# Performance work log

Hardware: AMD Instinct MI355X
Metric: run time of the kernel (lower is better)

Reference implementation:

```python
import jax, jax.numpy as jnp
import numpy as np

BINS = 10
MMT = 0.9
N = 33554432  # 2^25 elements


def setup_inputs() -> dict:
    key = jax.random.key(0)
    k1, k2, k3 = jax.random.split(key, 3)
    pred = jax.random.normal(k1, (N,), dtype=jnp.float32)
    target = jax.random.randint(k2, (N,), 0, 2, dtype=jnp.int32)
    acc_sum = jax.random.uniform(k3, (BINS,), dtype=jnp.float32)
    return {"pred": pred, "target": target, "acc_sum": acc_sum}


def reference(pred, target, acc_sum):
    bins = acc_sum.shape[0]
    # border = arange(bins+1)/bins, with last edge nudged up by 1e-6
    border = jnp.arange(bins + 1, dtype=jnp.float32) / bins
    border = border.at[-1].add(1e-6)

    t = target.astype(jnp.float32)
    # gradient density measure on detached predictions
    g = jnp.abs(jax.nn.sigmoid(jax.lax.stop_gradient(pred)) - t)
    # bin index: g in [border[i], border[i+1])  ->  i
    idx = jnp.clip(jnp.searchsorted(border, g, side='right') - 1, 0, bins - 1)

    # single-pass histogram (replaces the per-bin mask loop)
    counts = jax.ops.segment_sum(jnp.ones_like(g), idx, num_segments=bins)
    nonempty = counts > 0

    # momentum-accumulated bin statistics (only updated for non-empty bins)
    acc_new = jnp.where(nonempty, MMT * acc_sum + (1.0 - MMT) * counts, acc_sum)

    tot = jnp.float32(max(pred.shape[0], 1.0))
    safe_acc = jnp.where(nonempty, acc_new, 1.0)
    bin_w = jnp.where(nonempty, tot / safe_acc, 0.0)  # [bins]

    n = jnp.sum(nonempty.astype(jnp.float32))
    bin_w = jnp.where(n > 0, bin_w / jnp.maximum(n, 1.0), bin_w)

    # per-element GHM weights are constants w.r.t. pred (buffer + detached g)
    w = jax.lax.stop_gradient(bin_w[idx])

    # BCE-with-logits, numerically stable
    bce = jnp.maximum(pred, 0.0) - pred * t + jnp.log1p(jnp.exp(-jnp.abs(pred)))
    return jnp.sum(w * bce) / tot
```

## Files before the change

kernel.cpp:

```cpp
#include <hip/hip_runtime.h>

#define BINS 10
#define NTHREADS 256


__device__ __forceinline__ float wave_reduce_add(float v) {
#pragma unroll
    for (int off = 32; off > 0; off >>= 1) v += __shfl_down(v, off, 64);
    return v;
}
__device__ __forceinline__ unsigned int wave_reduce_addu(unsigned int v) {
#pragma unroll
    for (int off = 32; off > 0; off >>= 1) v += __shfl_down((int)v, off, 64);
    return v;
}

#define GHM_C1  2.19722458f
#define GHM_C2  1.38629436f
#define GHM_C3  0.84729786f
#define GHM_C4  0.40546511f
#define GHM_C5  0.0f
#define GHM_C6 -0.40546511f
#define GHM_C7 -0.84729786f
#define GHM_C8 -1.38629436f
#define GHM_C9 -2.19722458f
#define LOG2E 1.44269504f

__global__ __launch_bounds__(NTHREADS, 8) void ghm_pass1(
    const float* __restrict__ pred, const int* __restrict__ target,
    float* __restrict__ g_T,
    unsigned int* __restrict__ g_C,
    int n4, int n)
{
    float T[BINS];
    unsigned int cnt[BINS];
#pragma unroll
    for (int b = 0; b < BINS; ++b) { T[b] = 0.f; cnt[b] = 0u; }

    const float4* __restrict__ p4 = reinterpret_cast<const float4*>(pred);
    const int4*   __restrict__ t4 = reinterpret_cast<const int4*>(target);

    const int tid    = threadIdx.x;
    const int gtid   = blockIdx.x * NTHREADS + tid;
    const int stride = gridDim.x * NTHREADS;
    const int step   = 2 * stride;

#define GHM_BODY(xv, tv)                                                     \
    {                                                                        \
        const float xs_[4] = {(xv).x, (xv).y, (xv).z, (xv).w};               \
        const int   ts_[4] = {(tv).x, (tv).y, (tv).z, (tv).w};               \
        _Pragma("unroll")                                                    \
        for (int j = 0; j < 4; ++j) {                                        \
            const float x = xs_[j];                                          \
            const float y = (ts_[j] != 0) ? x : -x;                          \
            const float E = __builtin_amdgcn_exp2f(-y * LOG2E);              \
            const float bce2 = __builtin_amdgcn_logf(1.0f + E);              \
            T[0] += bce2;                                                    \
            { const bool p = (y <= GHM_C1); T[1]+=p?bce2:0.f; cnt[1]+=p; }   \
            { const bool p = (y <= GHM_C2); T[2]+=p?bce2:0.f; cnt[2]+=p; }   \
            { const bool p = (y <= GHM_C3); T[3]+=p?bce2:0.f; cnt[3]+=p; }   \
            { const bool p = (y <= GHM_C4); T[4]+=p?bce2:0.f; cnt[4]+=p; }   \
            { const bool p = (y <= GHM_C5); T[5]+=p?bce2:0.f; cnt[5]+=p; }   \
            { const bool p = (y <= GHM_C6); T[6]+=p?bce2:0.f; cnt[6]+=p; }   \
            { const bool p = (y <= GHM_C7); T[7]+=p?bce2:0.f; cnt[7]+=p; }   \
            { const bool p = (y <= GHM_C8); T[8]+=p?bce2:0.f; cnt[8]+=p; }   \
            { const bool p = (y <= GHM_C9); T[9]+=p?bce2:0.f; cnt[9]+=p; }   \
        }                                                                    \
    }

    const int R = (step > 0) ? (n4 / step) : 0;
    if (R > 0) {
        int idx = gtid;
        float4 xa0 = p4[idx];
        int4   ta0 = t4[idx];
        float4 xa1 = p4[idx + stride];
        int4   ta1 = t4[idx + stride];
        for (int r = 1; r < R; ++r) {
            const int nidx = gtid + r * step;
            const float4 xb0 = p4[nidx];
            const int4   tb0 = t4[nidx];
            const float4 xb1 = p4[nidx + stride];
            const int4   tb1 = t4[nidx + stride];
            GHM_BODY(xa0, ta0);
            GHM_BODY(xa1, ta1);
            xa0 = xb0; ta0 = tb0; xa1 = xb1; ta1 = tb1;
        }
        GHM_BODY(xa0, ta0);
        GHM_BODY(xa1, ta1);
    }
    for (int i = gtid + R * step; i < n4; i += stride) {
        const float4 xv = p4[i];
        const int4   tv = t4[i];
        GHM_BODY(xv, tv);
    }
    if (gtid == 0) {
        for (int i = n4 * 4; i < n; ++i) {
            const float x = pred[i];
            const float y = (target[i] != 0) ? x : -x;
            const float E = __builtin_amdgcn_exp2f(-y * LOG2E);
            const float bce2 = __builtin_amdgcn_logf(1.0f + E);
            T[0] += bce2;
            { const bool p = (y <= GHM_C1); T[1]+=p?bce2:0.f; cnt[1]+=p; }
            { const bool p = (y <= GHM_C2); T[2]+=p?bce2:0.f; cnt[2]+=p; }
            { const bool p = (y <= GHM_C3); T[3]+=p?bce2:0.f; cnt[3]+=p; }
            { const bool p = (y <= GHM_C4); T[4]+=p?bce2:0.f; cnt[4]+=p; }
            { const bool p = (y <= GHM_C5); T[5]+=p?bce2:0.f; cnt[5]+=p; }
            { const bool p = (y <= GHM_C6); T[6]+=p?bce2:0.f; cnt[6]+=p; }
            { const bool p = (y <= GHM_C7); T[7]+=p?bce2:0.f; cnt[7]+=p; }
            { const bool p = (y <= GHM_C8); T[8]+=p?bce2:0.f; cnt[8]+=p; }
            { const bool p = (y <= GHM_C9); T[9]+=p?bce2:0.f; cnt[9]+=p; }
        }
    }
#undef GHM_BODY

    __shared__ float        r_T[BINS];
    __shared__ unsigned int r_C[BINS];
    if (tid < BINS) { r_T[tid] = 0.f; r_C[tid] = 0u; }
    __syncthreads();

    const int lane = tid & 63;
#pragma unroll
    for (int b = 0; b < BINS; ++b) {
        const float        v = wave_reduce_add(T[b]);
        const unsigned int c = (b > 0) ? wave_reduce_addu(cnt[b]) : 0u;
        if (lane == 0) {
            atomicAdd(&r_T[b], v);
            if (b > 0) atomicAdd(&r_C[b], c);
        }
    }
    __syncthreads();

    if (tid < BINS) {
        atomicAdd(&g_T[tid], r_T[tid]);
        atomicAdd(&g_C[tid], r_C[tid]);
    }
}

__global__ void ghm_finalize(const float* __restrict__ g_T,
                             const unsigned int* __restrict__ g_C,
                             const float* __restrict__ acc_sum,
                             float* __restrict__ out, float tot, unsigned int ntot)
{
    if (threadIdx.x == 0 && blockIdx.x == 0) {
        const float LN2 = 0.69314718056f;
        float S[BINS];
        float cntf[BINS];
#pragma unroll
        for (int b = 0; b < BINS; ++b) {
            const float        Tc = g_T[b];
            const float        Tn = (b + 1 < BINS) ? g_T[b + 1] : 0.f;
            const unsigned int Cc = (b == 0) ? ntot : g_C[b];
            const unsigned int Cn = (b + 1 < BINS) ? g_C[b + 1] : 0u;
            S[b]    = (Tc - Tn) * LN2;
            cntf[b] = (float)(Cc - Cn);
        }
        float binw[BINS];
        int nne = 0;
#pragma unroll
        for (int b = 0; b < BINS; ++b) {
            const bool ne = (cntf[b] > 0.0f);
            const float accn = ne ? (0.9f * acc_sum[b] + 0.1f * cntf[b]) : acc_sum[b];
            binw[b] = ne ? (tot / accn) : 0.0f;
            nne += ne ? 1 : 0;
        }
        const float scale = (nne > 0) ? (1.0f / (float)nne) : 1.0f;
        float res = 0.0f;
#pragma unroll
        for (int b = 0; b < BINS; ++b) res += (binw[b] * scale) * S[b];
        out[0] = res / tot;
    }
}

extern "C" void kernel_launch(void* const* d_in, const int* in_sizes, int n_in,
                              void* d_out, int out_size, void* d_ws, size_t ws_size,
                              hipStream_t stream) {
    const float* pred    = (const float*)d_in[0];
    const int*   target  = (const int*)d_in[1];
    const float* acc_sum = (const float*)d_in[2];
    float*       out     = (float*)d_out;

    const int n  = in_sizes[0];
    const int n4 = n / 4;

    float*        g_T = (float*)d_ws;
    unsigned int* g_C = (unsigned int*)((float*)d_ws + BINS);

    hipMemsetAsync(d_ws, 0, 2 * BINS * sizeof(float), stream);

    ghm_pass1<<<2048, NTHREADS, 0, stream>>>(pred, target, g_T, g_C, n4, n);

    const float tot = (float)(n > 1 ? n : 1);
    ghm_finalize<<<1, 64, 0, stream>>>(g_T, g_C, acc_sum, out, tot, (unsigned int)n);
}
```

Baseline: 88.55 us.

## Pack bin counts into biased float sums and tile loads per block

```diff
diff --git a/kernel.cpp b/kernel.cpp
--- a/kernel.cpp
+++ b/kernel.cpp
@@ -2,7 +2,21 @@
 
 #define BINS 10
 #define NTHREADS 256
+#define LOG2E 1.44269504f
+#define KBIAS 1024.0f
+#define TILE_ELEMS (NTHREADS * 64)
+#define ROUNDS 8
 
+
+#define GHM_C1  2.19722458f
+#define GHM_C2  1.38629436f
+#define GHM_C3  0.84729786f
+#define GHM_C4  0.40546511f
+#define GHM_C5  0.0f
+#define GHM_C6 -0.40546511f
+#define GHM_C7 -0.84729786f
+#define GHM_C8 -1.38629436f
+#define GHM_C9 -2.19722458f
 
 __device__ __forceinline__ float wave_reduce_add(float v) {
 #pragma unroll
@@ -15,103 +29,83 @@
     return v;
 }
 
-#define GHM_C1  2.19722458f
-#define GHM_C2  1.38629436f
-#define GHM_C3  0.84729786f
-#define GHM_C4  0.40546511f
-#define GHM_C5  0.0f
-#define GHM_C6 -0.40546511f
-#define GHM_C7 -0.84729786f
-#define GHM_C8 -1.38629436f
-#define GHM_C9 -2.19722458f
-#define LOG2E 1.44269504f
-
-__global__ __launch_bounds__(NTHREADS, 8) void ghm_pass1(
+__global__ __launch_bounds__(NTHREADS, 6) void ghm_pass1(
     const float* __restrict__ pred, const int* __restrict__ target,
     float* __restrict__ g_T,
     unsigned int* __restrict__ g_C,
-    int n4, int n)
+    int n)
 {
-    float T[BINS];
-    unsigned int cnt[BINS];
+    float T0 = 0.f;
+    float Tb[9];
 #pragma unroll
-    for (int b = 0; b < BINS; ++b) { T[b] = 0.f; cnt[b] = 0u; }
-
-    const float4* __restrict__ p4 = reinterpret_cast<const float4*>(pred);
-    const int4*   __restrict__ t4 = reinterpret_cast<const int4*>(target);
+    for (int b = 0; b < 9; ++b) Tb[b] = 0.f;
 
     const int tid    = threadIdx.x;
-    const int gtid   = blockIdx.x * NTHREADS + tid;
-    const int stride = gridDim.x * NTHREADS;
-    const int step   = 2 * stride;
+    const int ntiles = n / TILE_ELEMS;
+
+#define GHM_ELEM(x_, t_)                                                     \
+    {                                                                        \
+        const float x = (x_);                                                \
+        const float y = ((t_) != 0) ? x : -x;                                \
+        const float E = __builtin_amdgcn_exp2f(y * -LOG2E);                  \
+        const float r1 = 1.0f + E;                                           \
+        const float bce2 = __builtin_amdgcn_logf(r1);                        \
+        const float ad = bce2 + KBIAS;                                       \
+        T0 += bce2;                                                          \
+        Tb[0] += (y <= GHM_C1) ? ad : 0.f;                                   \
+        Tb[1] += (y <= GHM_C2) ? ad : 0.f;                                   \
+        Tb[2] += (y <= GHM_C3) ? ad : 0.f;                                   \
+        Tb[3] += (y <= GHM_C4) ? ad : 0.f;                                   \
+        Tb[4] += (y <= GHM_C5) ? ad : 0.f;                                   \
+        Tb[5] += (y <= GHM_C6) ? ad : 0.f;                                   \
+        Tb[6] += (y <= GHM_C7) ? ad : 0.f;                                   \
+        Tb[7] += (y <= GHM_C8) ? ad : 0.f;                                   \
+        Tb[8] += (y <= GHM_C9) ? ad : 0.f;                                   \
+    }
 
 #define GHM_BODY(xv, tv)                                                     \
     {                                                                        \
-        const float xs_[4] = {(xv).x, (xv).y, (xv).z, (xv).w};               \
-        const int   ts_[4] = {(tv).x, (tv).y, (tv).z, (tv).w};               \
-        _Pragma("unroll")                                                    \
-        for (int j = 0; j < 4; ++j) {                                        \
-            const float x = xs_[j];                                          \
-            const float y = (ts_[j] != 0) ? x : -x;                          \
-            const float E = __builtin_amdgcn_exp2f(-y * LOG2E);              \
-            const float bce2 = __builtin_amdgcn_logf(1.0f + E);              \
-            T[0] += bce2;                                                    \
-            { const bool p = (y <= GHM_C1); T[1]+=p?bce2:0.f; cnt[1]+=p; }   \
-            { const bool p = (y <= GHM_C2); T[2]+=p?bce2:0.f; cnt[2]+=p; }   \
-            { const bool p = (y <= GHM_C3); T[3]+=p?bce2:0.f; cnt[3]+=p; }   \
-            { const bool p = (y <= GHM_C4); T[4]+=p?bce2:0.f; cnt[4]+=p; }   \
-            { const bool p = (y <= GHM_C5); T[5]+=p?bce2:0.f; cnt[5]+=p; }   \
-            { const bool p = (y <= GHM_C6); T[6]+=p?bce2:0.f; cnt[6]+=p; }   \
-            { const bool p = (y <= GHM_C7); T[7]+=p?bce2:0.f; cnt[7]+=p; }   \
-            { const bool p = (y <= GHM_C8); T[8]+=p?bce2:0.f; cnt[8]+=p; }   \
-            { const bool p = (y <= GHM_C9); T[9]+=p?bce2:0.f; cnt[9]+=p; }   \
-        }                                                                    \
+        GHM_ELEM((xv).x, (tv).x); GHM_ELEM((xv).y, (tv).y);                  \
+        GHM_ELEM((xv).z, (tv).z); GHM_ELEM((xv).w, (tv).w);                  \
     }
 
-    const int R = (step > 0) ? (n4 / step) : 0;
-    if (R > 0) {
-        int idx = gtid;
-        float4 xa0 = p4[idx];
-        int4   ta0 = t4[idx];
-        float4 xa1 = p4[idx + stride];
-        int4   ta1 = t4[idx + stride];
-        for (int r = 1; r < R; ++r) {
-            const int nidx = gtid + r * step;
-            const float4 xb0 = p4[nidx];
-            const int4   tb0 = t4[nidx];
-            const float4 xb1 = p4[nidx + stride];
-            const int4   tb1 = t4[nidx + stride];
+    for (int tile = blockIdx.x; tile < ntiles; tile += gridDim.x) {
+        const float4* __restrict__ p4 =
+            reinterpret_cast<const float4*>(pred) + (size_t)tile * (TILE_ELEMS / 4) + tid * 2;
+        const int4* __restrict__ t4 =
+            reinterpret_cast<const int4*>(target) + (size_t)tile * (TILE_ELEMS / 4) + tid * 2;
+
+        float4 xa0 = p4[0], xa1 = p4[1];
+        int4   ta0 = t4[0], ta1 = t4[1];
+        for (int r = 1; r < ROUNDS; ++r) {
+            const int o = r * (NTHREADS * 2);
+            const float4 xb0 = p4[o], xb1 = p4[o + 1];
+            const int4   tb0 = t4[o], tb1 = t4[o + 1];
             GHM_BODY(xa0, ta0);
             GHM_BODY(xa1, ta1);
-            xa0 = xb0; ta0 = tb0; xa1 = xb1; ta1 = tb1;
+            xa0 = xb0; xa1 = xb1; ta0 = tb0; ta1 = tb1;
         }
         GHM_BODY(xa0, ta0);
         GHM_BODY(xa1, ta1);
     }
-    for (int i = gtid + R * step; i < n4; i += stride) {
-        const float4 xv = p4[i];
-        const int4   tv = t4[i];
-        GHM_BODY(xv, tv);
-    }
-    if (gtid == 0) {
-        for (int i = n4 * 4; i < n; ++i) {
-            const float x = pred[i];
-            const float y = (target[i] != 0) ? x : -x;
-            const float E = __builtin_amdgcn_exp2f(-y * LOG2E);
-            const float bce2 = __builtin_amdgcn_logf(1.0f + E);
-            T[0] += bce2;
-            { const bool p = (y <= GHM_C1); T[1]+=p?bce2:0.f; cnt[1]+=p; }
-            { const bool p = (y <= GHM_C2); T[2]+=p?bce2:0.f; cnt[2]+=p; }
-            { const bool p = (y <= GHM_C3); T[3]+=p?bce2:0.f; cnt[3]+=p; }
-            { const bool p = (y <= GHM_C4); T[4]+=p?bce2:0.f; cnt[4]+=p; }
-            { const bool p = (y <= GHM_C5); T[5]+=p?bce2:0.f; cnt[5]+=p; }
-            { const bool p = (y <= GHM_C6); T[6]+=p?bce2:0.f; cnt[6]+=p; }
-            { const bool p = (y <= GHM_C7); T[7]+=p?bce2:0.f; cnt[7]+=p; }
-            { const bool p = (y <= GHM_C8); T[8]+=p?bce2:0.f; cnt[8]+=p; }
-            { const bool p = (y <= GHM_C9); T[9]+=p?bce2:0.f; cnt[9]+=p; }
+
+    if (blockIdx.x == gridDim.x - 1) {
+        for (int i = ntiles * TILE_ELEMS + tid; i < n; i += NTHREADS) {
+            GHM_ELEM(pred[i], target[i]);
         }
     }
 #undef GHM_BODY
+#undef GHM_ELEM
+
+    float        sums[BINS];
+    unsigned int cnts[BINS];
+    sums[0] = T0; cnts[0] = 0u;
+#pragma unroll
+    for (int b = 1; b < BINS; ++b) {
+        const float cf = floorf(Tb[b - 1] * (1.0f / KBIAS));
+        cnts[b] = (unsigned int)cf;
+        sums[b] = Tb[b - 1] - KBIAS * cf;
+    }
 
     __shared__ float        r_T[BINS];
     __shared__ unsigned int r_C[BINS];
@@ -121,8 +115,8 @@
     const int lane = tid & 63;
 #pragma unroll
     for (int b = 0; b < BINS; ++b) {
-        const float        v = wave_reduce_add(T[b]);
-        const unsigned int c = (b > 0) ? wave_reduce_addu(cnt[b]) : 0u;
+        const float        v = wave_reduce_add(sums[b]);
+        const unsigned int c = (b > 0) ? wave_reduce_addu(cnts[b]) : 0u;
         if (lane == 0) {
             atomicAdd(&r_T[b], v);
             if (b > 0) atomicAdd(&r_C[b], c);
@@ -179,15 +173,14 @@
     const float* acc_sum = (const float*)d_in[2];
     float*       out     = (float*)d_out;
 
-    const int n  = in_sizes[0];
-    const int n4 = n / 4;
+    const int n = in_sizes[0];
 
     float*        g_T = (float*)d_ws;
     unsigned int* g_C = (unsigned int*)((float*)d_ws + BINS);
 
     hipMemsetAsync(d_ws, 0, 2 * BINS * sizeof(float), stream);
 
-    ghm_pass1<<<2048, NTHREADS, 0, stream>>>(pred, target, g_T, g_C, n4, n);
+    ghm_pass1<<<2048, NTHREADS, 0, stream>>>(pred, target, g_T, g_C, n);
 
     const float tot = (float)(n > 1 ? n : 1);
     ghm_finalize<<<1, 64, 0, stream>>>(g_T, g_C, acc_sum, out, tot, (unsigned int)n);
```

New measurement: 90.20 us. About the same (+1.9%).
